# Performance work log

Measured on AMD Instinct MI355X. Metric: run time of the kernel, lower is better.

The kernel has to match this reference:

```python
import jax, jax.numpy as jnp
import numpy as np

N_CODES = 16384
EMB_DIM = 256
BETA = 0.25


def setup_inputs() -> dict:
    key = jax.random.key(0)
    k1, k2 = jax.random.split(key)
    z = jax.random.normal(k1, (8, EMB_DIM, 32, 32), dtype=jnp.float32)
    # embedding init: uniform(-1/n_codes, 1/n_codes)
    emb = jax.random.uniform(k2, (N_CODES, EMB_DIM), dtype=jnp.float32,
                             minval=-1.0 / N_CODES, maxval=1.0 / N_CODES)
    return {"z": z, "emb": emb}


def reference(z, emb):
    # z: [B, C, H, W] -> [B, H, W, C]
    z_nhwc = jnp.transpose(z, (0, 2, 3, 1))
    zf = z_nhwc.reshape(-1, EMB_DIM)  # [N, D]
    # squared distances ||z||^2 + ||e||^2 - 2 z.e   -> [N, n_codes]
    d = (jnp.sum(zf * zf, axis=1, keepdims=True)
         + jnp.sum(emb * emb, axis=1)
         - 2.0 * jnp.einsum('nd,kd->nk', zf, emb))
    idx = jnp.argmin(d, axis=1)  # [N]
    z_q = emb[idx].reshape(z_nhwc.shape)  # [B, H, W, C]
    sg = jax.lax.stop_gradient
    loss = jnp.mean((sg(z_q) - z_nhwc) ** 2) + BETA * jnp.mean((z_q - sg(z_nhwc)) ** 2)
    # straight-through estimator
    z_q = z_nhwc + sg(z_q - z_nhwc)
    z_q = jnp.transpose(z_q, (0, 3, 1, 2))  # back to NCHW
    return z_q, loss, idx
```

## Files before the change

kernel.cpp:

```cpp
#include <hip/hip_runtime.h>
#include <hip/hip_fp16.h>

#define DIM 256
#define MARGIN 2.25e-4f

typedef __bf16 bf8v __attribute__((ext_vector_type(8)));
typedef float f4v __attribute__((ext_vector_type(4)));

__device__ inline unsigned short f2bf(float x) {
    unsigned u = __float_as_uint(x);
    u += 0x7fffu + ((u >> 16) & 1u);
    return (unsigned short)(u >> 16);
}

__global__ __launch_bounds__(256) void k_prep(const float* __restrict__ z,
                                              const float* __restrict__ emb,
                                              float* __restrict__ zf,
                                              unsigned short* __restrict__ zb,
                                              unsigned short* __restrict__ eb,
                                              float* __restrict__ enorm,
                                              float* __restrict__ out_loss) {
    const int bx = blockIdx.x;
    if (bx < 2048) {
        __shared__ float tt[32][33];
        const int hw0 = (bx & 31) * 32;
        const int d0  = ((bx >> 5) & 7) * 32;
        const int b   = bx >> 8;
        const int tx = threadIdx.x & 31, ty = threadIdx.x >> 5;
#pragma unroll
        for (int i = 0; i < 4; i++) {
            const int d = d0 + ty + 8 * i;
            tt[ty + 8 * i][tx] = z[(b * 256 + d) * 1024 + hw0 + tx];
        }
        __syncthreads();
#pragma unroll
        for (int i = 0; i < 4; i++) {
            const int hw = hw0 + ty + 8 * i;
            const float v = tt[tx][ty + 8 * i];
            const size_t o = (size_t)(b * 1024 + hw) * DIM + d0 + tx;
            zf[o] = v;
            zb[o] = f2bf(v);
        }
    } else if (bx < 6144) {
        const int s = bx - 2048;
        const int wave = threadIdx.x >> 6, lane = threadIdx.x & 63;
        const int row = s * 4 + wave;
        const float4 v = *(const float4*)(emb + (size_t)row * DIM + lane * 4);
        ushort4 o;
        o.x = f2bf(v.x); o.y = f2bf(v.y); o.z = f2bf(v.z); o.w = f2bf(v.w);
        const int g = row >> 4, m = row & 15;
        const int kk = lane >> 3, qq = (lane >> 1) & 3, e = (lane & 1) * 4;
        *(ushort4*)(eb + (size_t)(g * 8 + kk) * 512 + qq * 128 + m * 8 + e) = o;
        float ss = v.x * v.x + v.y * v.y + v.z * v.z + v.w * v.w;
#pragma unroll
        for (int m2 = 1; m2 < 64; m2 <<= 1) ss += __shfl_xor(ss, m2, 64);
        if (lane == 0) enorm[row] = ss;
    } else {
        if (threadIdx.x == 0) out_loss[0] = 0.f;
    }
}

#define GLOADB(dst, voff, base) \
    asm volatile("global_load_dwordx4 %0, %1, %2" : "=&v"(dst) : "v"(voff), "s"(base))
#define SO(KK) ((unsigned)((((KK) >> 3) * 131072) + (((KK) & 7) * 1024)))

#define ISSUE(sl, KK) \
    GLOADB(Bp##sl##_0, voffb0 + SO(KK), eb); \
    GLOADB(Bp##sl##_1, voffb1 + SO(KK), eb); \
    GLOADB(Bp##sl##_2, voffb2 + SO(KK), eb); \
    GLOADB(Bp##sl##_3, voffb3 + SO(KK), eb);

#define MFMA4(rt, AF, sl) \
    acc[rt][0] = __builtin_amdgcn_mfma_f32_16x16x32_bf16(AF, Bp##sl##_0, acc[rt][0], 0, 0, 0); \
    acc[rt][1] = __builtin_amdgcn_mfma_f32_16x16x32_bf16(AF, Bp##sl##_1, acc[rt][1], 0, 0, 0); \
    acc[rt][2] = __builtin_amdgcn_mfma_f32_16x16x32_bf16(AF, Bp##sl##_2, acc[rt][2], 0, 0, 0); \
    acc[rt][3] = __builtin_amdgcn_mfma_f32_16x16x32_bf16(AF, Bp##sl##_3, acc[rt][3], 0, 0, 0);

#define PF(dp, kk) { \
    const int slot_ = (((kk) * 4 + q) ^ m15) * 8; \
    Af##dp##_0 = *(const bf8v*)&As[(m15)      * 256 + slot_]; \
    Af##dp##_1 = *(const bf8v*)&As[(16 + m15) * 256 + slot_]; \
    Af##dp##_2 = *(const bf8v*)&As[(32 + m15) * 256 + slot_]; \
    Af##dp##_3 = *(const bf8v*)&As[(48 + m15) * 256 + slot_]; }

#define CMP(P, sl) \
    __builtin_amdgcn_s_setprio(1); \
    MFMA4(0, Af##P##_0, sl) \
    MFMA4(1, Af##P##_1, sl) \
    MFMA4(2, Af##P##_2, sl) \
    MFMA4(3, Af##P##_3, sl) \
    __builtin_amdgcn_s_setprio(0);

#define WV(n) { asm volatile("s_waitcnt vmcnt(" #n ")" ::: "memory"); \
                __builtin_amdgcn_sched_barrier(0); }
#define SB __builtin_amdgcn_sched_barrier(0);

#define EPI(pp) { \
    const int by_ = nb * 4 + (pp); \
    const int gsl_ = wc * 4 + (m15 >> 2); \
    const float e0_ = en_lds[(pp) * 256 + wc * 64 +  0 + m15]; \
    const float e1_ = en_lds[(pp) * 256 + wc * 64 + 16 + m15]; \
    const float e2_ = en_lds[(pp) * 256 + wc * 64 + 32 + m15]; \
    const float e3_ = en_lds[(pp) * 256 + wc * 64 + 48 + m15]; \
    _Pragma("unroll") \
    for (int rt = 0; rt < 4; rt++) { \
        float sv[4]; \
        _Pragma("unroll") \
        for (int j = 0; j < 4; j++) { \
            float s_ = fmaf(-2.f, acc[rt][0][j], e0_); \
            s_ = fminf(s_, fmaf(-2.f, acc[rt][1][j], e1_)); \
            s_ = fminf(s_, fmaf(-2.f, acc[rt][2][j], e2_)); \
            s_ = fminf(s_, fmaf(-2.f, acc[rt][3][j], e3_)); \
            sv[j] = s_; \
        } \
        _Pragma("unroll") \
        for (int m = 1; m <= 2; m <<= 1) { \
            _Pragma("unroll") \
            for (int j = 0; j < 4; j++) sv[j] = fminf(sv[j], __shfl_xor(sv[j], m, 64)); \
        } \
        if ((m15 & 3) == 0) { \
            const int rl_ = rt * 16 + q * 4; \
            _Pragma("unroll") \
            for (int j = 0; j < 4; j++) \
                sm[(rl_ + j) * 16 + gsl_] = __half_as_ushort(__float2half_rn(sv[j])); \
        } \
    } \
    asm volatile("s_waitcnt lgkmcnt(0)" ::: "memory"); \
    __builtin_amdgcn_sched_barrier(0); \
    __builtin_amdgcn_s_barrier(); \
    __builtin_amdgcn_sched_barrier(0); \
    if (t < 128) { \
        const uint4 v_ = *(const uint4*)&sm[t * 8]; \
        *(uint4*)&pvalh[(size_t)(row0 + (t >> 1)) * 1024 + by_ * 16 + (t & 1) * 8] = v_; \
    } \
    __builtin_amdgcn_sched_barrier(0); \
    __builtin_amdgcn_s_barrier(); \
    __builtin_amdgcn_sched_barrier(0); \
    _Pragma("unroll") \
    for (int rt = 0; rt < 4; rt++) { \
        _Pragma("unroll") \
        for (int ct = 0; ct < 4; ct++) acc[rt][ct] = (f4v){0.f, 0.f, 0.f, 0.f}; \
    } }

__global__ __launch_bounds__(256, 3) void k_score(
        const unsigned short* __restrict__ zb, const unsigned short* __restrict__ eb,
        const float* __restrict__ enorm, unsigned short* __restrict__ pvalh) {
    __shared__ unsigned short As[64 * 256];
    __shared__ unsigned short sm[64 * 16];
    __shared__ float en_lds[1024];
    const int bid = blockIdx.x;
    const int rx = (bid >> 3) & 127;
    const int nb = ((bid >> 10) << 3) + (bid & 7);
    const int row0 = rx * 64;
    const int t = threadIdx.x;
    const int lane = t & 63, wc = t >> 6;
    const int q = lane >> 4, m15 = lane & 15;

#pragma unroll
    for (int j = 0; j < 8; j++) {
        const int id = j * 256 + t;
        const int r = id >> 5, sl = id & 31;
        const int c = sl ^ (r & 15);
        __builtin_amdgcn_global_load_lds(
            (const __attribute__((address_space(1))) void*)(zb + (size_t)(row0 + r) * DIM + c * 8),
            (__attribute__((address_space(3))) void*)((char*)As + id * 16), 16, 0, 0);
    }
#pragma unroll
    for (int j = 0; j < 4; j++) {
        __builtin_amdgcn_global_load_lds(
            (const __attribute__((address_space(1))) void*)(enorm + nb * 1024 + j * 256 + t),
            (__attribute__((address_space(3))) void*)((char*)en_lds + (j * 256 + t) * 4), 4, 0, 0);
    }
    __syncthreads();

    f4v acc[4][4];
#pragma unroll
    for (int rt = 0; rt < 4; rt++)
#pragma unroll
        for (int ct = 0; ct < 4; ct++) acc[rt][ct] = (f4v){0.f, 0.f, 0.f, 0.f};

    const unsigned voffb0 = (unsigned)((nb * 64 + wc * 4 + 0) * 8192 + lane * 16);
    const unsigned voffb1 = (unsigned)((nb * 64 + wc * 4 + 1) * 8192 + lane * 16);
    const unsigned voffb2 = (unsigned)((nb * 64 + wc * 4 + 2) * 8192 + lane * 16);
    const unsigned voffb3 = (unsigned)((nb * 64 + wc * 4 + 3) * 8192 + lane * 16);

    bf8v Bp0_0, Bp0_1, Bp0_2, Bp0_3;
    bf8v Bp1_0, Bp1_1, Bp1_2, Bp1_3;
    bf8v Af0_0, Af0_1, Af0_2, Af0_3;
    bf8v Af1_0, Af1_1, Af1_2, Af1_3;

    ISSUE(0, 0) ISSUE(1, 1)
    PF(0, 0)

    WV(4) PF(1, 1) SB CMP(0, 0) ISSUE(0, 2)
    WV(4) PF(0, 2) SB CMP(1, 1) ISSUE(1, 3)
    WV(4) PF(1, 3) SB CMP(0, 0) ISSUE(0, 4)
    WV(4) PF(0, 4) SB CMP(1, 1) ISSUE(1, 5)
    WV(4) PF(1, 5) SB CMP(0, 0) ISSUE(0, 6)
    WV(4) PF(0, 6) SB CMP(1, 1) ISSUE(1, 7)
    WV(4) PF(1, 7) SB CMP(0, 0) ISSUE(0, 8)
    WV(4) PF(0, 0) SB CMP(1, 1) ISSUE(1, 9)
    EPI(0)
    WV(4) PF(1, 1) SB CMP(0, 0) ISSUE(0, 10)
    WV(4) PF(0, 2) SB CMP(1, 1) ISSUE(1, 11)
    WV(4) PF(1, 3) SB CMP(0, 0) ISSUE(0, 12)
    WV(4) PF(0, 4) SB CMP(1, 1) ISSUE(1, 13)
    WV(4) PF(1, 5) SB CMP(0, 0) ISSUE(0, 14)
    WV(4) PF(0, 6) SB CMP(1, 1) ISSUE(1, 15)
    WV(4) PF(1, 7) SB CMP(0, 0) ISSUE(0, 16)
    WV(4) PF(0, 0) SB CMP(1, 1) ISSUE(1, 17)
    EPI(1)
    WV(4) PF(1, 1) SB CMP(0, 0) ISSUE(0, 18)
    WV(4) PF(0, 2) SB CMP(1, 1) ISSUE(1, 19)
    WV(4) PF(1, 3) SB CMP(0, 0) ISSUE(0, 20)
    WV(4) PF(0, 4) SB CMP(1, 1) ISSUE(1, 21)
    WV(4) PF(1, 5) SB CMP(0, 0) ISSUE(0, 22)
    WV(4) PF(0, 6) SB CMP(1, 1) ISSUE(1, 23)
    WV(4) PF(1, 7) SB CMP(0, 0) ISSUE(0, 24)
    WV(4) PF(0, 0) SB CMP(1, 1) ISSUE(1, 25)
    EPI(2)
    WV(4) PF(1, 1) SB CMP(0, 0) ISSUE(0, 26)
    WV(4) PF(0, 2) SB CMP(1, 1) ISSUE(1, 27)
    WV(4) PF(1, 3) SB CMP(0, 0) ISSUE(0, 28)
    WV(4) PF(0, 4) SB CMP(1, 1) ISSUE(1, 29)
    WV(4) PF(1, 5) SB CMP(0, 0) ISSUE(0, 30)
    WV(4) PF(0, 6) SB CMP(1, 1) ISSUE(1, 31)
    WV(4) PF(1, 7) SB CMP(0, 0)
    WV(0)          SB CMP(1, 1)
    EPI(3)
}

__global__ __launch_bounds__(256) void k_select(
        const float* __restrict__ zf, const float* __restrict__ emb,
        const float* __restrict__ enorm, const unsigned short* __restrict__ pvalh,
        int* __restrict__ idxi, float* __restrict__ out_idx) {
    const int row = blockIdx.x;
    const int t = threadIdx.x;
    const int lane = t & 63, w = t >> 6;
    __shared__ float zs[256];
    __shared__ float wred[4];
    __shared__ int lcnt;
    __shared__ int list[1024];
    __shared__ float fs[16];
    __shared__ int fi[16];

    const float zv = zf[(size_t)row * DIM + t];
    zs[t] = zv;
    if (t == 0) lcnt = 0;
    float nrm = zv * zv;
#pragma unroll
    for (int m = 1; m < 64; m <<= 1) nrm += __shfl_xor(nrm, m, 64);
    if (lane == 0) wred[w] = nrm;

    const __half* p = (const __half*)(pvalh + (size_t)row * 1024 + t * 4);
    float v[4];
#pragma unroll
    for (int k = 0; k < 4; k++) v[k] = __half2float(p[k]);
    float mn = fminf(fminf(v[0], v[1]), fminf(v[2], v[3]));
#pragma unroll
    for (int m = 1; m < 64; m <<= 1) mn = fminf(mn, __shfl_xor(mn, m, 64));
    __shared__ float wmin[4];
    if (lane == 0) wmin[w] = mn;
    __syncthreads();
    const float zn = wred[0] + wred[1] + wred[2] + wred[3];
    const float g = fminf(fminf(wmin[0], wmin[1]), fminf(wmin[2], wmin[3])) + MARGIN;
#pragma unroll
    for (int k = 0; k < 4; k++) {
        if (v[k] <= g) {
            const int pos = atomicAdd(&lcnt, 1);
            list[pos] = t * 4 + k;
        }
    }
    __syncthreads();

    const int lane16 = t & 15, codei = t >> 4;
    const int n = lcnt;
    float bv = 3.0e38f;
    int bi = 0x7fffffff;
    for (int i = 0; i < n; i++) {
        const int gg = list[i];
        const int cbase = ((gg >> 4) << 8) + (((gg >> 2) & 3) << 6) + ((gg & 3) << 2);
        const int code = cbase + ((codei >> 2) << 4) + (codei & 3);
        const float* zp = zs + lane16 * 16;
        const float* ep = emb + (size_t)code * DIM + lane16 * 16;
        float d = 0.f;
#pragma unroll
        for (int k = 0; k < 16; k += 4) {
            const float4 ev = *(const float4*)(ep + k);
            const float4 zv4 = *(const float4*)(zp + k);
            d = fmaf(zv4.x, ev.x, d);
            d = fmaf(zv4.y, ev.y, d);
            d = fmaf(zv4.z, ev.z, d);
            d = fmaf(zv4.w, ev.w, d);
        }
#pragma unroll
        for (int m = 1; m <= 8; m <<= 1) d += __shfl_xor(d, m, 64);
        if (lane16 == 0) {
            const float tt = zn + enorm[code];
            const float s = tt - 2.0f * d;
            if (s < bv || (s == bv && code < bi)) { bv = s; bi = code; }
        }
    }
    if (lane16 == 0) { fs[codei] = bv; fi[codei] = bi; }
    __syncthreads();
    if (t == 0) {
        float b = fs[0]; int c = fi[0];
#pragma unroll
        for (int k = 1; k < 16; k++)
            if (fs[k] < b || (fs[k] == b && fi[k] < c)) { b = fs[k]; c = fi[k]; }
        idxi[row] = c;
        out_idx[row] = (float)c;
    }
}

__global__ __launch_bounds__(256) void k_gather(const float* __restrict__ emb,
                                                const float* __restrict__ zf,
                                                const int* __restrict__ idxi,
                                                float* __restrict__ zq,
                                                float* __restrict__ out_loss) {
    __shared__ float t[32][33];
    const int hw0 = blockIdx.x * 32;
    const int c0  = blockIdx.y * 32;
    const int b   = blockIdx.z;
    const int tx = threadIdx.x & 31, ty = threadIdx.x >> 5;
    float lsum = 0.f;
#pragma unroll
    for (int i = 0; i < 4; i++) {
        const int hh = ty + 8 * i;
        const int n = b * 1024 + hw0 + hh;
        const int id = idxi[n];
        const float q = emb[(size_t)id * DIM + c0 + tx];
        const float zv = zf[(size_t)n * DIM + c0 + tx];
        const float d = q - zv;
        lsum += d * d;
        t[hh][tx] = q;
    }
    __syncthreads();
#pragma unroll
    for (int i = 0; i < 4; i++) {
        const int c = c0 + ty + 8 * i;
        zq[(size_t)(b * 256 + c) * 1024 + hw0 + tx] = t[tx][ty + 8 * i];
    }
#pragma unroll
    for (int m = 1; m < 64; m <<= 1) lsum += __shfl_xor(lsum, m, 64);
    __shared__ float wsum[4];
    const int lane = threadIdx.x & 63, w = threadIdx.x >> 6;
    if (lane == 0) wsum[w] = lsum;
    __syncthreads();
    if (threadIdx.x == 0) {
        const float total = wsum[0] + wsum[1] + wsum[2] + wsum[3];
        atomicAdd(out_loss, total * (1.25f / 2097152.0f));
    }
}

extern "C" void kernel_launch(void* const* d_in, const int* in_sizes, int n_in,
                              void* d_out, int out_size, void* d_ws, size_t ws_size,
                              hipStream_t stream) {
    const float* z   = (const float*)d_in[0];
    const float* emb = (const float*)d_in[1];
    float* out = (float*)d_out;
    float* ws  = (float*)d_ws;

    float*          zf    = ws;
    unsigned short* pvalh = (unsigned short*)(ws + 2097152);
    unsigned short* zb    = (unsigned short*)(ws + 6291456);
    unsigned short* eb    = (unsigned short*)(ws + 7340032);
    float*          enorm = ws + 9437184;
    int*            idxi  = (int*)(ws + 9453568);

    float* zq       = out;
    float* out_loss = out + 2097152;
    float* out_idx  = out + 2097153;

    k_prep<<<dim3(6145), 256, 0, stream>>>(z, emb, zf, zb, eb, enorm, out_loss);
    k_score<<<dim3(2048), 256, 0, stream>>>(zb, eb, enorm, pvalh);
    k_select<<<dim3(8192), 256, 0, stream>>>(zf, emb, enorm, pvalh, idxi, out_idx);
    k_gather<<<dim3(32, 8, 8), 256, 0, stream>>>(emb, zf, idxi, zq, out_loss);
}
```

Baseline: 215.9 us.

## Coarsen prep, select and gather kernels to process more work per block

Three kernels are coarsened. In the embedding-prep path each block now converts 16 rows instead of 4. k_select handles two rows per block, with both rows' loads issued up front so their latency overlaps. k_gather processes four channel tiles per block and reuses the loaded indices across them. The aim is to cut block launch and scheduling overhead and to hide load latency, at the cost of fewer blocks, extra barriers and less parallelism to hide the serial per-row select loop.

```diff
diff --git a/kernel.cpp b/kernel.cpp
--- a/kernel.cpp
+++ b/kernel.cpp
@@ -41,20 +41,23 @@
             zf[o] = v;
             zb[o] = f2bf(v);
         }
-    } else if (bx < 6144) {
-        const int s = bx - 2048;
+    } else if (bx < 3072) {
+        const int s2 = bx - 2048;
         const int wave = threadIdx.x >> 6, lane = threadIdx.x & 63;
-        const int row = s * 4 + wave;
-        const float4 v = *(const float4*)(emb + (size_t)row * DIM + lane * 4);
-        ushort4 o;
-        o.x = f2bf(v.x); o.y = f2bf(v.y); o.z = f2bf(v.z); o.w = f2bf(v.w);
-        const int g = row >> 4, m = row & 15;
-        const int kk = lane >> 3, qq = (lane >> 1) & 3, e = (lane & 1) * 4;
-        *(ushort4*)(eb + (size_t)(g * 8 + kk) * 512 + qq * 128 + m * 8 + e) = o;
-        float ss = v.x * v.x + v.y * v.y + v.z * v.z + v.w * v.w;
-#pragma unroll
-        for (int m2 = 1; m2 < 64; m2 <<= 1) ss += __shfl_xor(ss, m2, 64);
-        if (lane == 0) enorm[row] = ss;
+#pragma unroll
+        for (int j = 0; j < 4; j++) {
+            const int row = s2 * 16 + j * 4 + wave;
+            const float4 v = *(const float4*)(emb + (size_t)row * DIM + lane * 4);
+            ushort4 o;
+            o.x = f2bf(v.x); o.y = f2bf(v.y); o.z = f2bf(v.z); o.w = f2bf(v.w);
+            const int g = row >> 4, m = row & 15;
+            const int kk = lane >> 3, qq = (lane >> 1) & 3, e = (lane & 1) * 4;
+            *(ushort4*)(eb + (size_t)(g * 8 + kk) * 512 + qq * 128 + m * 8 + e) = o;
+            float ss = v.x * v.x + v.y * v.y + v.z * v.z + v.w * v.w;
+#pragma unroll
+            for (int m2 = 1; m2 < 64; m2 <<= 1) ss += __shfl_xor(ss, m2, 64);
+            if (lane == 0) enorm[row] = ss;
+        }
     } else {
         if (threadIdx.x == 0) out_loss[0] = 0.f;
     }
@@ -230,11 +233,75 @@
     EPI(3)
 }
 
+#define SELROW(row, zvv, pu) { \
+    zs[t] = (zvv); \
+    if (t == 0) lcnt = 0; \
+    float nrm = (zvv) * (zvv); \
+    _Pragma("unroll") \
+    for (int m = 1; m < 64; m <<= 1) nrm += __shfl_xor(nrm, m, 64); \
+    if (lane == 0) wred[w] = nrm; \
+    float v[4]; \
+    _Pragma("unroll") \
+    for (int k = 0; k < 4; k++) v[k] = __half2float(((const __half*)&(pu))[k]); \
+    float mn = fminf(fminf(v[0], v[1]), fminf(v[2], v[3])); \
+    _Pragma("unroll") \
+    for (int m = 1; m < 64; m <<= 1) mn = fminf(mn, __shfl_xor(mn, m, 64)); \
+    if (lane == 0) wmin[w] = mn; \
+    __syncthreads(); \
+    const float zn = wred[0] + wred[1] + wred[2] + wred[3]; \
+    const float g = fminf(fminf(wmin[0], wmin[1]), fminf(wmin[2], wmin[3])) + MARGIN; \
+    _Pragma("unroll") \
+    for (int k = 0; k < 4; k++) { \
+        if (v[k] <= g) { \
+            const int pos = atomicAdd(&lcnt, 1); \
+            list[pos] = t * 4 + k; \
+        } \
+    } \
+    __syncthreads(); \
+    const int lane16 = t & 15, codei = t >> 4; \
+    const int n = lcnt; \
+    float bv = 3.0e38f; \
+    int bi = 0x7fffffff; \
+    for (int i = 0; i < n; i++) { \
+        const int gg = list[i]; \
+        const int cbase = ((gg >> 4) << 8) + (((gg >> 2) & 3) << 6) + ((gg & 3) << 2); \
+        const int code = cbase + ((codei >> 2) << 4) + (codei & 3); \
+        const float* zp = zs + lane16 * 16; \
+        const float* ep = emb + (size_t)code * DIM + lane16 * 16; \
+        float d = 0.f; \
+        _Pragma("unroll") \
+        for (int k = 0; k < 16; k += 4) { \
+            const float4 ev = *(const float4*)(ep + k); \
+            const float4 zv4 = *(const float4*)(zp + k); \
+            d = fmaf(zv4.x, ev.x, d); \
+            d = fmaf(zv4.y, ev.y, d); \
+            d = fmaf(zv4.z, ev.z, d); \
+            d = fmaf(zv4.w, ev.w, d); \
+        } \
+        _Pragma("unroll") \
+        for (int m = 1; m <= 8; m <<= 1) d += __shfl_xor(d, m, 64); \
+        if (lane16 == 0) { \
+            const float tt = zn + enorm[code]; \
+            const float s = tt - 2.0f * d; \
+            if (s < bv || (s == bv && code < bi)) { bv = s; bi = code; } \
+        } \
+    } \
+    if (lane16 == 0) { fs[codei] = bv; fi[codei] = bi; } \
+    __syncthreads(); \
+    if (t == 0) { \
+        float b = fs[0]; int c = fi[0]; \
+        _Pragma("unroll") \
+        for (int k = 1; k < 16; k++) \
+            if (fs[k] < b || (fs[k] == b && fi[k] < c)) { b = fs[k]; c = fi[k]; } \
+        idxi[row] = c; \
+        out_idx[row] = (float)c; \
+    } \
+    __syncthreads(); }
+
 __global__ __launch_bounds__(256) void k_select(
         const float* __restrict__ zf, const float* __restrict__ emb,
         const float* __restrict__ enorm, const unsigned short* __restrict__ pvalh,
         int* __restrict__ idxi, float* __restrict__ out_idx) {
-    const int row = blockIdx.x;
     const int t = threadIdx.x;
     const int lane = t & 63, w = t >> 6;
     __shared__ float zs[256];
@@ -243,74 +310,17 @@
     __shared__ int list[1024];
     __shared__ float fs[16];
     __shared__ int fi[16];
-
-    const float zv = zf[(size_t)row * DIM + t];
-    zs[t] = zv;
-    if (t == 0) lcnt = 0;
-    float nrm = zv * zv;
-#pragma unroll
-    for (int m = 1; m < 64; m <<= 1) nrm += __shfl_xor(nrm, m, 64);
-    if (lane == 0) wred[w] = nrm;
-
-    const __half* p = (const __half*)(pvalh + (size_t)row * 1024 + t * 4);
-    float v[4];
-#pragma unroll
-    for (int k = 0; k < 4; k++) v[k] = __half2float(p[k]);
-    float mn = fminf(fminf(v[0], v[1]), fminf(v[2], v[3]));
-#pragma unroll
-    for (int m = 1; m < 64; m <<= 1) mn = fminf(mn, __shfl_xor(mn, m, 64));
     __shared__ float wmin[4];
-    if (lane == 0) wmin[w] = mn;
-    __syncthreads();
-    const float zn = wred[0] + wred[1] + wred[2] + wred[3];
-    const float g = fminf(fminf(wmin[0], wmin[1]), fminf(wmin[2], wmin[3])) + MARGIN;
-#pragma unroll
-    for (int k = 0; k < 4; k++) {
-        if (v[k] <= g) {
-            const int pos = atomicAdd(&lcnt, 1);
-            list[pos] = t * 4 + k;
-        }
-    }
-    __syncthreads();
-
-    const int lane16 = t & 15, codei = t >> 4;
-    const int n = lcnt;
-    float bv = 3.0e38f;
-    int bi = 0x7fffffff;
-    for (int i = 0; i < n; i++) {
-        const int gg = list[i];
-        const int cbase = ((gg >> 4) << 8) + (((gg >> 2) & 3) << 6) + ((gg & 3) << 2);
-        const int code = cbase + ((codei >> 2) << 4) + (codei & 3);
-        const float* zp = zs + lane16 * 16;
-        const float* ep = emb + (size_t)code * DIM + lane16 * 16;
-        float d = 0.f;
-#pragma unroll
-        for (int k = 0; k < 16; k += 4) {
-            const float4 ev = *(const float4*)(ep + k);
-            const float4 zv4 = *(const float4*)(zp + k);
-            d = fmaf(zv4.x, ev.x, d);
-            d = fmaf(zv4.y, ev.y, d);
-            d = fmaf(zv4.z, ev.z, d);
-            d = fmaf(zv4.w, ev.w, d);
-        }
-#pragma unroll
-        for (int m = 1; m <= 8; m <<= 1) d += __shfl_xor(d, m, 64);
-        if (lane16 == 0) {
-            const float tt = zn + enorm[code];
-            const float s = tt - 2.0f * d;
-            if (s < bv || (s == bv && code < bi)) { bv = s; bi = code; }
-        }
-    }
-    if (lane16 == 0) { fs[codei] = bv; fi[codei] = bi; }
-    __syncthreads();
-    if (t == 0) {
-        float b = fs[0]; int c = fi[0];
-#pragma unroll
-        for (int k = 1; k < 16; k++)
-            if (fs[k] < b || (fs[k] == b && fi[k] < c)) { b = fs[k]; c = fi[k]; }
-        idxi[row] = c;
-        out_idx[row] = (float)c;
-    }
+
+    const int r0 = blockIdx.x, r1 = blockIdx.x + 4096;
+    const float zv0 = zf[(size_t)r0 * DIM + t];
+    const float zv1 = zf[(size_t)r1 * DIM + t];
+    const uint2 pu0 = *(const uint2*)(pvalh + (size_t)r0 * 1024 + t * 4);
+    const uint2 pu1 = *(const uint2*)(pvalh + (size_t)r1 * 1024 + t * 4);
+    asm volatile("" :: "v"(zv0), "v"(zv1), "v"(pu0.x), "v"(pu0.y), "v"(pu1.x), "v"(pu1.y));
+
+    SELROW(r0, zv0, pu0)
+    SELROW(r1, zv1, pu1)
 }
 
 __global__ __launch_bounds__(256) void k_gather(const float* __restrict__ emb,
@@ -320,26 +330,33 @@
                                                 float* __restrict__ out_loss) {
     __shared__ float t[32][33];
     const int hw0 = blockIdx.x * 32;
-    const int c0  = blockIdx.y * 32;
+    const int c0g = blockIdx.y * 128;
     const int b   = blockIdx.z;
     const int tx = threadIdx.x & 31, ty = threadIdx.x >> 5;
     float lsum = 0.f;
-#pragma unroll
-    for (int i = 0; i < 4; i++) {
-        const int hh = ty + 8 * i;
-        const int n = b * 1024 + hw0 + hh;
-        const int id = idxi[n];
-        const float q = emb[(size_t)id * DIM + c0 + tx];
-        const float zv = zf[(size_t)n * DIM + c0 + tx];
-        const float d = q - zv;
-        lsum += d * d;
-        t[hh][tx] = q;
-    }
-    __syncthreads();
-#pragma unroll
-    for (int i = 0; i < 4; i++) {
-        const int c = c0 + ty + 8 * i;
-        zq[(size_t)(b * 256 + c) * 1024 + hw0 + tx] = t[tx][ty + 8 * i];
+    int ids[4];
+#pragma unroll
+    for (int i = 0; i < 4; i++) ids[i] = idxi[b * 1024 + hw0 + ty + 8 * i];
+#pragma unroll
+    for (int j = 0; j < 4; j++) {
+        const int c0 = c0g + j * 32;
+#pragma unroll
+        for (int i = 0; i < 4; i++) {
+            const int hh = ty + 8 * i;
+            const int n = b * 1024 + hw0 + hh;
+            const float q = emb[(size_t)ids[i] * DIM + c0 + tx];
+            const float zv = zf[(size_t)n * DIM + c0 + tx];
+            const float d = q - zv;
+            lsum += d * d;
+            t[hh][tx] = q;
+        }
+        __syncthreads();
+#pragma unroll
+        for (int i = 0; i < 4; i++) {
+            const int c = c0 + ty + 8 * i;
+            zq[(size_t)(b * 256 + c) * 1024 + hw0 + tx] = t[tx][ty + 8 * i];
+        }
+        __syncthreads();
     }
 #pragma unroll
     for (int m = 1; m < 64; m <<= 1) lsum += __shfl_xor(lsum, m, 64);
@@ -372,8 +389,8 @@
     float* out_loss = out + 2097152;
     float* out_idx  = out + 2097153;
 
-    k_prep<<<dim3(6145), 256, 0, stream>>>(z, emb, zf, zb, eb, enorm, out_loss);
+    k_prep<<<dim3(3073), 256, 0, stream>>>(z, emb, zf, zb, eb, enorm, out_loss);
     k_score<<<dim3(2048), 256, 0, stream>>>(zb, eb, enorm, pvalh);
-    k_select<<<dim3(8192), 256, 0, stream>>>(zf, emb, enorm, pvalh, idxi, out_idx);
-    k_gather<<<dim3(32, 8, 8), 256, 0, stream>>>(emb, zf, idxi, zq, out_loss);
-}
+    k_select<<<dim3(4096), 256, 0, stream>>>(zf, emb, enorm, pvalh, idxi, out_idx);
+    k_gather<<<dim3(32, 2, 8), 256, 0, stream>>>(emb, zf, idxi, zq, out_loss);
+}
```

Result: faster. 201.0 us (-6.9%).
